# Optimization experiments

Hardware: AMD Instinct MI355X
Metric: run time of the kernel (lower is better)

The kernel has to match this reference:

```python
import jax, jax.numpy as jnp
import numpy as np

S, B, T = 400, 32, 32          # encoder seq len, batch, max_summary_length
V, OOV, E, H = 50000, 50, 128, 256


def _p(key, shape, scale=0.05):
    return (jax.random.normal(key, shape) * scale).astype(jnp.float32)


def lstm_step(x, h, c, Wih, Whh, bih, bhh):
    # PyTorch LSTM gate order: i, f, g, o
    g = x @ Wih.T + h @ Whh.T + bih + bhh
    i, f, gg, o = jnp.split(g, 4, axis=-1)
    c = jax.nn.sigmoid(f) * c + jax.nn.sigmoid(i) * jnp.tanh(gg)
    h = jax.nn.sigmoid(o) * jnp.tanh(c)
    return h, c


def setup_inputs() -> dict:
    key = jax.random.key(0)
    ks = jax.random.split(key, 34)
    inp = {
        # token ids >= 1 so encoder_mask = clip(inputs,0,1) is all ones and
        # packed lengths == full length (PackedRNN becomes a plain LSTM)
        "inputs": jax.random.randint(ks[0], (S, B), 1, V),
        "inputs_lengths": jnp.full((B,), S, dtype=jnp.int32),
        "outputs_tokens": jax.random.randint(ks[1], (T, B), 1, V),  # teacher-forced targets
        "texts_extended": jax.random.randint(ks[2], (S, B), 1, V + OOV),
        "oov_size": OOV,
        # learned parameters
        "embedding": _p(ks[3], (V, E)).at[0].set(0.0),  # padding_idx=0
        "enc_Wih_f": _p(ks[4], (4 * H, E)), "enc_Whh_f": _p(ks[5], (4 * H, H)),
        "enc_bih_f": _p(ks[6], (4 * H,)), "enc_bhh_f": _p(ks[7], (4 * H,)),
        "enc_Wih_b": _p(ks[8], (4 * H, E)), "enc_Whh_b": _p(ks[9], (4 * H, H)),
        "enc_bih_b": _p(ks[10], (4 * H,)), "enc_bhh_b": _p(ks[11], (4 * H,)),
        "W_feat": _p(ks[12], (2 * H, 2 * H)),  # encoder.features (no bias)
        "W_rh": _p(ks[13], (H, 2 * H)), "b_rh": _p(ks[14], (H,)),
        "W_rc": _p(ks[15], (H, 2 * H)), "b_rc": _p(ks[16], (H,)),
        "W_af": _p(ks[17], (2 * H, 2 * H)), "b_af": _p(ks[18], (2 * H,)),  # attention.features
        "w_v": _p(ks[19], (2 * H,)),  # attention_first Linear(2H,1,no bias)
        "W_ctx": _p(ks[20], (E, 2 * H + E)), "b_ctx": _p(ks[21], (E,)),  # decoder.context
        "dec_Wih": _p(ks[22], (4 * H, E)), "dec_Whh": _p(ks[23], (4 * H, H)),
        "dec_bih": _p(ks[24], (4 * H,)), "dec_bhh": _p(ks[25], (4 * H,)),
        "W_pg": _p(ks[26], (1, 4 * H + E)), "b_pg": _p(ks[27], (1,)),
        "W_o1": _p(ks[28], (H, 4 * H)), "b_o1": _p(ks[29], (H,)),
        "W_o2": _p(ks[30], (V, H)), "b_o2": _p(ks[31], (V,)),
    }
    return inp


def reference(inputs, inputs_lengths, outputs_tokens, texts_extended, oov_size,
              embedding, enc_Wih_f, enc_Whh_f, enc_bih_f, enc_bhh_f,
              enc_Wih_b, enc_Whh_b, enc_bih_b, enc_bhh_b,
              W_feat, W_rh, b_rh, W_rc, b_rc, W_af, b_af, w_v,
              W_ctx, b_ctx, dec_Wih, dec_Whh, dec_bih, dec_bhh,
              W_pg, b_pg, W_o1, b_o1, W_o2, b_o2):
    Bsz = inputs.shape[1]
    emb_in = embedding[inputs]                                # [S,B,E]
    h0 = jnp.zeros((Bsz, H), jnp.float32)

    # --- bidirectional encoder LSTM (lengths == S, so packing is a no-op) ---
    def enc_f(carry, x):
        h, c = carry
        h, c = lstm_step(x, h, c, enc_Wih_f, enc_Whh_f, enc_bih_f, enc_bhh_f)
        return (h, c), h

    def enc_b(carry, x):
        h, c = carry
        h, c = lstm_step(x, h, c, enc_Wih_b, enc_Whh_b, enc_bih_b, enc_bhh_b)
        return (h, c), h

    (hf, cf), out_f = jax.lax.scan(enc_f, (h0, h0), emb_in)
    (hb, cb), out_b = jax.lax.scan(enc_b, (h0, h0), emb_in[::-1])
    out_b = out_b[::-1]
    enc_out = jnp.concatenate([out_f, out_b], -1)             # [S,B,2H]
    enc_feat = enc_out @ W_feat.T                             # [S,B,2H]
    dh0 = jax.nn.relu(jnp.concatenate([hf, hb], -1) @ W_rh.T + b_rh)  # [B,H]
    dc0 = jax.nn.relu(jnp.concatenate([cf, cb], -1) @ W_rc.T + b_rc)  # [B,H]

    mask = jnp.clip(inputs, 0, 1).astype(jnp.float32)          # [S,B]
    ctx0 = jnp.zeros((Bsz, 2 * H), jnp.float32)
    rows = jnp.arange(Bsz)[:, None]
    tex_T = texts_extended.T                                   # [B,S]

    # --- decoder loop (teacher forcing, coverage disabled: default) ---
    def dec_step(carry, tok):
        h, c, ctx = carry
        x = jnp.concatenate([ctx, embedding[tok]], 1) @ W_ctx.T + b_ctx     # [B,E]
        h, c = lstm_step(x, h, c, dec_Wih, dec_Whh, dec_bih, dec_bhh)
        dh = jnp.concatenate([h, c], 1)                                      # [B,2H]
        e = jnp.tanh(enc_feat + (dh @ W_af.T + b_af)[None]) @ w_v            # [S,B]
        a = jax.nn.softmax(e, axis=0) * mask
        a = a / a.sum(0, keepdims=True)                                      # layers.Normalize(0)
        context = jnp.einsum('sb,sbd->bd', a, enc_out)                       # [B,2H]
        p_gen = jax.nn.sigmoid(jnp.concatenate([context, dh, x], 1) @ W_pg.T + b_pg)  # [B,1]
        hid = jnp.concatenate([dh, context], 1) @ W_o1.T + b_o1              # [B,H]
        out_v = jax.nn.softmax(hid @ W_o2.T + b_o2, axis=1)                  # [B,V]
        vd = jnp.pad(p_gen * out_v, ((0, 0), (0, oov_size)))                 # [B,V+OOV]
        final = vd.at[rows, tex_T].add((1.0 - p_gen) * a.T)                  # scatter_add copy dist
        return (h, c, context), (final, a)

    _, (outs, atts) = jax.lax.scan(dec_step, (dh0, dc0, ctx0), outputs_tokens)
    return outs, atts  # [T,B,V+OOV], [T,S,B]
```

## Files before the change

### kernel.cpp

```cpp
#include <hip/hip_runtime.h>

#define DEV static __device__ __forceinline__

typedef short  s16x8 __attribute__((ext_vector_type(8)));
typedef float  f32x4 __attribute__((ext_vector_type(4)));
typedef _Float16 h2f __attribute__((ext_vector_type(2)));

constexpr int S = 400, B = 32, T = 32, V = 50000, OOV = 50, E = 128, H = 256;
constexpr int VO = V + OOV, SB = S * B;
constexpr int VP = 50048;

DEV ushort f2bf(float x) {
    union { float f; unsigned u; } a; a.f = x;
    unsigned r = (a.u + 0x7fffu + ((a.u >> 16) & 1u)) >> 16;
    return (ushort)r;
}
DEV float bf2f(unsigned b) {
    union { unsigned u; float f; } a; a.u = b << 16; return a.f;
}
DEV float sigmoidf_(float x) { return 1.0f / (1.0f + __expf(-x)); }
DEV float tanhf_(float x) { float e = __expf(2.0f * x); return 1.0f - 2.0f / (e + 1.0f); }
DEV h2f asH2(unsigned u) { union { unsigned u; h2f h; } x; x.u = u; return x.h; }

#if __has_builtin(__builtin_amdgcn_fdot2)
DEV float dot2(h2f a, h2f b, float c) { return __builtin_amdgcn_fdot2(a, b, c, false); }
#else
DEV float dot2(h2f a, h2f b, float c) { return c + (float)a.x * (float)b.x + (float)a.y * (float)b.y; }
#endif

DEV unsigned f2e4(float v) {
    union { float f; unsigned u; } a; a.f = v;
    unsigned u = a.u + 0x0007FFFFu + ((a.u >> 20) & 1u);
    int e = (int)((u >> 23) & 255) - 127 + 7;
    unsigned m = (u >> 20) & 7u;
    if (e <= 0) return 0u;
    if (e > 15) { e = 15; m = 6; }
    return (unsigned)((e << 3) | m);
}
DEV float e42f(unsigned b) {
    int e = (int)((b >> 3) & 15), m = (int)(b & 7);
    if (e == 0) return (float)m * 1.953125e-3f;
    union { unsigned u; float f; } a;
    a.u = ((unsigned)(e + 120) << 23) | ((unsigned)m << 20);
    return a.f;
}

constexpr size_t SZ_EMB2D  = (size_t)SB * E * 2;
constexpr size_t SZ_WIHCAT = (size_t)2048 * 128 * 2;
constexpr size_t SZ_BIASX  = 2048 * 4;
constexpr size_t SZ_WFEAT  = (size_t)512 * 512 * 2;
constexpr size_t SZ_WO2    = (size_t)V * H * 2;
constexpr size_t SZ_WHH2   = (size_t)2 * 64 * 512 * 16;
constexpr size_t SZ_WCAT   = (size_t)1024 * 896 * 4;
constexpr size_t SZ_BC     = 1024 * 4;
constexpr size_t SZ_CPG    = 256;
constexpr size_t SZ_WRHT   = (size_t)512 * 256 * 4;
constexpr size_t SZ_WRCT   = (size_t)512 * 256 * 4;
constexpr size_t SZ_EMBDEC = (size_t)T * B * E * 4;
constexpr size_t SZ_WZ     = 1664 * 4 + 256;
constexpr size_t SZ_WAFBF  = (size_t)512 * 512 * 2;
constexpr size_t SZ_WO1BF  = (size_t)256 * 1024 * 2;
constexpr size_t SZ_CTXACC = (size_t)(T + 2) * 16384 * 4;
constexpr size_t SZ_SSUM   = (size_t)(T + 2) * 32 * 4 + 256;
constexpr size_t SZ_XALL   = (size_t)T * B * 1024 * 2;
constexpr size_t SZ_EXPS   = (size_t)T * SB * 4;
constexpr size_t SZ_XPROJ  = (size_t)SB * 2048 * 2;
constexpr size_t SZ_ENCOUT = (size_t)SB * 512 * 2;
constexpr size_t SZ_ENCFEAT= (size_t)SB * 512 * 2;
constexpr size_t SZ_HFIN   = (size_t)2 * B * H * 4;
constexpr size_t SZ_HPP    = (size_t)2 * B * H * 4;
constexpr size_t SZ_PGEN   = (size_t)T * B * 4;
constexpr size_t SZ_HIDALL = (size_t)T * B * 256 * 2;

constexpr size_t OFF_EMB2D  = 0;
constexpr size_t OFF_WIHCAT = OFF_EMB2D  + SZ_EMB2D;
constexpr size_t OFF_BIASX  = OFF_WIHCAT + SZ_WIHCAT;
constexpr size_t OFF_WFEAT  = OFF_BIASX  + SZ_BIASX;
constexpr size_t OFF_WO2    = OFF_WFEAT  + SZ_WFEAT;
constexpr size_t OFF_WHH2   = OFF_WO2    + SZ_WO2;
constexpr size_t OFF_WCAT   = OFF_WHH2   + SZ_WHH2;
constexpr size_t OFF_BC     = OFF_WCAT   + SZ_WCAT;
constexpr size_t OFF_CPG    = OFF_BC     + SZ_BC;
constexpr size_t OFF_WRHT   = OFF_CPG    + SZ_CPG;
constexpr size_t OFF_WRCT   = OFF_WRHT   + SZ_WRHT;
constexpr size_t OFF_EMBDEC = OFF_WRCT   + SZ_WRCT;
constexpr size_t OFF_WZ     = OFF_EMBDEC + SZ_EMBDEC;
constexpr size_t OFF_WAFBF  = OFF_WZ     + SZ_WZ;
constexpr size_t OFF_WO1BF  = OFF_WAFBF  + SZ_WAFBF;
constexpr size_t OFF_CTXACC = OFF_WO1BF  + SZ_WO1BF;
constexpr size_t OFF_SSUM   = OFF_CTXACC + SZ_CTXACC;
constexpr size_t OFF_XALL   = OFF_SSUM   + SZ_SSUM;
constexpr size_t OFF_EXPS   = OFF_XALL   + SZ_XALL;
constexpr size_t OFF_XPROJ  = OFF_EXPS   + SZ_EXPS;
constexpr size_t OFF_ENCOUT = OFF_XPROJ  + SZ_XPROJ;
constexpr size_t OFF_ENCFEAT= OFF_ENCOUT + SZ_ENCOUT;
constexpr size_t OFF_HFIN   = OFF_ENCFEAT+ SZ_ENCFEAT;
constexpr size_t OFF_CFIN   = OFF_HFIN   + SZ_HFIN;
constexpr size_t OFF_HPP    = OFF_CFIN   + SZ_HFIN;
constexpr size_t OFF_CPP    = OFF_HPP    + SZ_HPP;
constexpr size_t OFF_PGEN   = OFF_CPP    + SZ_HPP;
constexpr size_t OFF_HIDALL = OFF_PGEN   + SZ_PGEN;
constexpr size_t OFF_PBUF   = OFF_XPROJ;

constexpr long P1 = 2048L*128;
constexpr long P2 = 2048;
constexpr long P3 = 512L*512;
constexpr long P4 = (long)V*H;
constexpr long P5 = 2L*64*512*4;
constexpr long P6 = 1024L*896;
constexpr long P7 = 1;
constexpr long P8 = 1024;
constexpr long P9 = (long)SB*E;
constexpr long P10 = 512L*256;
constexpr long P11 = 512L*256;
constexpr long P12 = 32L*32*128;
constexpr long P13 = 1664;
constexpr long P14 = 512L*512;
constexpr long P15 = 256L*1024;
constexpr long P16 = (long)(T+2)*16384;
constexpr long P17 = (long)(T+2)*32;
constexpr long PREP_TOTAL = P1+P2+P3+P4+P5+P6+P7+P8+P9+P10+P11+P12+P13+P14+P15+P16+P17;

__global__ __launch_bounds__(256)
void prep_kernel(const float* __restrict__ Wih_f, const float* __restrict__ Wih_b,
                 const float* __restrict__ bih_f, const float* __restrict__ bhh_f,
                 const float* __restrict__ bih_b, const float* __restrict__ bhh_b,
                 const float* __restrict__ W_feat, const float* __restrict__ W_o2,
                 const float* __restrict__ Whh_f, const float* __restrict__ Whh_b,
                 const float* __restrict__ dWih, const float* __restrict__ W_ctx,
                 const float* __restrict__ W_pg, const float* __restrict__ b_pg,
                 const float* __restrict__ b_ctx, const float* __restrict__ dbih,
                 const float* __restrict__ dbhh, const float* __restrict__ emb,
                 const int* __restrict__ inputs, const float* __restrict__ dWhh,
                 const float* __restrict__ W_rh, const float* __restrict__ W_rc,
                 const int* __restrict__ toks, const float* __restrict__ W_af,
                 const float* __restrict__ W_o1,
                 ushort* __restrict__ emb2d, ushort* __restrict__ wihcat,
                 float* __restrict__ biasx, ushort* __restrict__ wfeatbf,
                 ushort* __restrict__ wo2bf, unsigned* __restrict__ whh2,
                 float* __restrict__ wcat, float* __restrict__ cpgp,
                 float* __restrict__ bcv, float* __restrict__ wrhT,
                 float* __restrict__ wrcT, float* __restrict__ embdec,
                 float* __restrict__ wz, ushort* __restrict__ wafbf,
                 ushort* __restrict__ wo1bf, float* __restrict__ ctxAcc,
                 float* __restrict__ ssumAll)
{
    long id = (long)blockIdx.x * 256 + threadIdx.x;
    if (id < P1) { int r = id >> 7, e = id & 127;
        float v = (r < 1024) ? Wih_f[r*128+e] : Wih_b[(r-1024)*128+e];
        wihcat[id] = f2bf(v); return; }
    id -= P1;
    if (id < P2) { biasx[id] = (id < 1024) ? bih_f[id]+bhh_f[id] : bih_b[id-1024]+bhh_b[id-1024]; return; }
    id -= P2;
    if (id < P3) { wfeatbf[id] = f2bf(W_feat[id]); return; }
    id -= P3;
    if (id < P4) { wo2bf[id] = f2bf(W_o2[id]); return; }
    id -= P4;
    if (id < P5) {
        int q = id & 3; long r = id >> 2;
        int t = (int)(r & 511); r >>= 9; int c = (int)(r & 63); int dir = (int)(r >> 6);
        int gate = c >> 4, p = c & 15, kh = t & 1;
        int j = t >> 1;
        int k0 = kh * 128 + p * 8 + 2 * q;
        int row = gate * 256 + j;
        const float* W = dir ? Whh_b : Whh_f;
        h2f hv; hv.x = (_Float16)W[(size_t)row*256 + k0]; hv.y = (_Float16)W[(size_t)row*256 + k0 + 1];
        whh2[id] = __builtin_bit_cast(unsigned, hv); return; }
    id -= P5;
    if (id < P6) { int col = (int)(id / 896), k = (int)(id % 896);
        if (k < 640) {
            float acc = 0.f;
            for (int e = 0; e < 128; ++e) acc += dWih[col*128+e] * W_ctx[e*640+k];
            wcat[id] = acc;
        } else wcat[id] = dWhh[(size_t)col*256 + (k - 640)];
        return; }
    id -= P6;
    if (id < P7) { float acc = b_pg[0];
        for (int e = 0; e < 128; ++e) acc += W_pg[1024+e] * b_ctx[e];
        cpgp[0] = acc; return; }
    id -= P7;
    if (id < P8) { float acc = dbih[id] + dbhh[id];
        for (int e = 0; e < 128; ++e) acc += dWih[id*128+e] * b_ctx[e];
        bcv[id] = acc; return; }
    id -= P8;
    if (id < P9) { long sb = id >> 7; int e = id & 127;
        emb2d[id] = f2bf(emb[(size_t)inputs[sb]*128 + e]); return; }
    id -= P9;
    if (id < P10) { int j = id & 255; long k = id >> 8;
        wrhT[id] = W_rh[(size_t)j * 512 + k]; return; }
    id -= P10;
    if (id < P11) { int j = id & 255; long k = id >> 8;
        wrcT[id] = W_rc[(size_t)j * 512 + k]; return; }
    id -= P11;
    if (id < P12) { long tb = id >> 7; int e = id & 127;
        embdec[id] = emb[(size_t)toks[tb]*128 + e]; return; }
    id -= P12;
    if (id < P13) {
        int k = (int)id;
        if (k < 1024) wz[k] = W_pg[k];
        else { int u = k - 1024; float acc = 0.f;
            for (int e = 0; e < 128; ++e) acc += W_pg[1024+e] * W_ctx[e*640+u];
            wz[k] = acc; }
        return; }
    id -= P13;
    if (id < P14) { int d = id & 511; long k = id >> 9;
        wafbf[id] = f2bf(W_af[(size_t)d * 512 + k]); return; }
    id -= P14;
    if (id < P15) { wo1bf[id] = f2bf(W_o1[id]); return; }
    id -= P15;
    if (id < P16) { ctxAcc[id] = 0.f; return; }
    id -= P16;
    if (id < P17) { ssumAll[id] = (id < 64) ? 1.0f : 0.f; return; }
}

template<int BM, int BN, int NT, int MODE, bool BIAS, bool SWZ>
__global__ __launch_bounds__(NT)
void gemm_nt(const ushort* __restrict__ A, int lda, const ushort* __restrict__ Bm, int ldb,
             void* __restrict__ Cp, int ldc, const float* __restrict__ bias,
             int M, int N, int K)
{
    constexpr int WN = BN / 32;
    __shared__ ushort sA[BM * 32];
    __shared__ ushort sB[BN * 32];
    int tid = threadIdx.x, lane = tid & 63, wid = tid >> 6;
    int wm = wid / WN, wn = wid % WN;
    int mb = blockIdx.y, nb = blockIdx.x;
    if (SWZ) {
        int n = gridDim.x, x = nb & 7, y = nb >> 3, q = n >> 3, r = n & 7;
// ... 66 lines not shown
    for (int c = 46; c < 64; ++c) wlds[(c - 46) * 512 + t] = gw[(size_t)c * 512];
    if (t < 256) { hh16[0][t >> 7][t & 127] = 0; }
    float cst = 0.f, hst = 0.f;
    __syncthreads();
    const int khoff = kh * 512;
    #pragma unroll 1
    for (int step = 0; step < S; ++step) {
        int s = dir ? (S - 1 - step) : step;
        int cur = step & 1, nxt = cur ^ 1;
        const ushort* xp = xproj + ((size_t)(s * B + b)) * 2048 + dir * 1024 + j + khoff;
        ushort xra = xp[0], xrb = xp[256];
        float a0 = 0.f, a1 = 0.f, a2 = 0.f, a3 = 0.f;
        #pragma unroll
        for (int p = 0; p < 16; ++p) {
            uint4 hp = *(const uint4*)(&hh16[cur][kh][p * 8]);
            uint4 wi = wreg[p];
            uint4 wf = wreg[16 + p];
            uint4 wg = (p < 14) ? wreg[32 + p] : wlds[(p - 14) * 512 + t];
            uint4 wo = wlds[(p + 2) * 512 + t];
            h2f p0 = asH2(hp.x), p1 = asH2(hp.y), p2 = asH2(hp.z), p3 = asH2(hp.w);
            a0 = dot2(p0, asH2(wi.x), a0); a0 = dot2(p1, asH2(wi.y), a0);
            a0 = dot2(p2, asH2(wi.z), a0); a0 = dot2(p3, asH2(wi.w), a0);
            a1 = dot2(p0, asH2(wf.x), a1); a1 = dot2(p1, asH2(wf.y), a1);
            a1 = dot2(p2, asH2(wf.z), a1); a1 = dot2(p3, asH2(wf.w), a1);
            a2 = dot2(p0, asH2(wg.x), a2); a2 = dot2(p1, asH2(wg.y), a2);
            a2 = dot2(p2, asH2(wg.z), a2); a2 = dot2(p3, asH2(wg.w), a2);
            a3 = dot2(p0, asH2(wo.x), a3); a3 = dot2(p1, asH2(wo.y), a3);
            a3 = dot2(p2, asH2(wo.z), a3); a3 = dot2(p3, asH2(wo.w), a3);
        }
        float xv0 = (float)__builtin_bit_cast(_Float16, xra);
        float xv1 = (float)__builtin_bit_cast(_Float16, xrb);
        a0 += kh ? 0.f : xv0;  a1 += kh ? 0.f : xv1;
        a2 += kh ? xv0 : 0.f;  a3 += kh ? xv1 : 0.f;
        a0 += __shfl_xor(a0, 1); a1 += __shfl_xor(a1, 1);
        a2 += __shfl_xor(a2, 1); a3 += __shfl_xor(a3, 1);
        cst = sigmoidf_(a1) * cst + sigmoidf_(a0) * tanhf_(a2);
        hst = sigmoidf_(a3) * tanhf_(cst);
        if (kh == 0) {
            encoutB[((size_t)(b * S + s)) * 512 + dir * 256 + j] = f2bf(hst);
            hh16[nxt][j >> 7][j & 127] = __builtin_bit_cast(ushort, (_Float16)hst);
        }
        __syncthreads();
    }
    if (kh == 0) {
        hfin[(dir * 32 + b) * 256 + j] = hst;
        cfin[(dir * 32 + b) * 256 + j] = cst;
    }
}

__global__ __launch_bounds__(256)
void initdec_kernel(const float* __restrict__ hfin, const float* __restrict__ cfin,
                    const float* __restrict__ wrhT, const float* __restrict__ b_rh,
                    const float* __restrict__ wrcT, const float* __restrict__ b_rc,
                    float* __restrict__ hPP, float* __restrict__ cPP)
{
    int b = blockIdx.x, j = threadIdx.x;
    float ah = b_rh[j], ac = b_rc[j];
    for (int k = 0; k < 512; ++k) {
        float hv = (k < 256) ? hfin[b * 256 + k] : hfin[(32 + b) * 256 + k - 256];
        float cv = (k < 256) ? cfin[b * 256 + k] : cfin[(32 + b) * 256 + k - 256];
        ah += hv * wrhT[k * 256 + j];
        ac += cv * wrcT[k * 256 + j];
    }
    hPP[b * 256 + j] = fmaxf(ah, 0.f);
    cPP[b * 256 + j] = fmaxf(ac, 0.f);
}

__global__ __launch_bounds__(256)
void dec_lstm2_kernel(const float* __restrict__ wcat, const float* __restrict__ bcv,
                      const float* __restrict__ ctxPrevAcc, const float* __restrict__ ssumPrev,
                      const float* __restrict__ hin, const float* __restrict__ cin,
                      float* __restrict__ hout, float* __restrict__ cout,
                      const float* __restrict__ embt, ushort* __restrict__ xAll_t)
{
    __shared__ float pre[256];
    int blk = blockIdx.x, tid = threadIdx.x;
    int b = tid & 31, ci = tid >> 5;
    int gi = ci >> 1, jj = ci & 1;
    int j = (blk << 1) + jj;
    int col = gi * 256 + j;
    float rinvb = 1.0f / ssumPrev[b];
    float acc = bcv[col], accC = 0.f;
    const float4* w = (const float4*)(wcat + (size_t)col * 896);
    const float4* x0 = (const float4*)(ctxPrevAcc + b * 512);
    #pragma unroll 8
    for (int u = 0; u < 128; ++u) { float4 a = w[u], q = x0[u]; accC += a.x*q.x + a.y*q.y + a.z*q.z + a.w*q.w; }
    const float4* x1 = (const float4*)(embt + b * 128);
    #pragma unroll 8
    for (int u = 0; u < 32; ++u) { float4 a = w[128 + u], q = x1[u]; acc += a.x*q.x + a.y*q.y + a.z*q.z + a.w*q.w; }
    const float4* x2 = (const float4*)(hin + b * 256);
    #pragma unroll 8
    for (int u = 0; u < 64; ++u) { float4 a = w[160 + u], q = x2[u]; acc += a.x*q.x + a.y*q.y + a.z*q.z + a.w*q.w; }
    pre[tid] = acc + rinvb * accC;
    __syncthreads();
    if (tid < 64) {
        int b2 = tid & 31, qq = tid >> 5;
        int j2 = (blk << 1) + qq;
        float iv = pre[(0 + qq) * 32 + b2];
        float fv = pre[(2 + qq) * 32 + b2];
        float gv = pre[(4 + qq) * 32 + b2];
        float ov = pre[(6 + qq) * 32 + b2];
        float cp = cin[b2 * 256 + j2];
        float cn = sigmoidf_(fv) * cp + sigmoidf_(iv) * tanhf_(gv);
        float hn = sigmoidf_(ov) * tanhf_(cn);
        cout[b2 * 256 + j2] = cn;
        hout[b2 * 256 + j2] = hn;
        xAll_t[(size_t)b2 * 1024 + j2] = f2bf(hn);
        xAll_t[(size_t)b2 * 1024 + 256 + j2] = f2bf(cn);
    }
}

__global__ __launch_bounds__(512)
void dec_attn2_kernel(const float* __restrict__ h, const float* __restrict__ c,
                      const ushort* __restrict__ wafbf, const float* __restrict__ b_af,
                      const ushort* __restrict__ encfeatB, const float* __restrict__ wv,
                      const int* __restrict__ inputs, const ushort* __restrict__ encoutB,
                      float* __restrict__ expsT, float* __restrict__ ssumT,
                      float* __restrict__ ctxAccT)
{
    __shared__ float hc[512];
    __shared__ float dafL[512];
    __shared__ float scL[50];
    __shared__ float part8[8][512];
    int blk = blockIdx.x, tid = threadIdx.x;
    int b = blk >> 3, sc = blk & 7, s0 = sc * 50;
    int sl = tid >> 6, dth = tid & 63;
    hc[tid] = (tid < 256) ? h[b * 256 + tid] : c[b * 256 + tid - 256];
    __syncthreads();
    {
        float acc8[8] = {};
        const ushort* wbase = wafbf + (size_t)(sl * 64) * 512 + dth * 8;
        #pragma unroll 8
        for (int kk = 0; kk < 64; ++kk) {
            uint4 u = *(const uint4*)(wbase + (size_t)kk * 512);
            float hk = hc[sl * 64 + kk];
            acc8[0] += hk * bf2f(u.x & 0xffffu);
            acc8[1] += hk * bf2f(u.x >> 16);
            acc8[2] += hk * bf2f(u.y & 0xffffu);
            acc8[3] += hk * bf2f(u.y >> 16);
            acc8[4] += hk * bf2f(u.z & 0xffffu);
            acc8[5] += hk * bf2f(u.z >> 16);
            acc8[6] += hk * bf2f(u.w & 0xffffu);
            acc8[7] += hk * bf2f(u.w >> 16);
        }
        #pragma unroll
        for (int jj = 0; jj < 8; ++jj) part8[sl][dth * 8 + jj] = acc8[jj];
    }
    __syncthreads();
    {
        float v = b_af[tid];
        #pragma unroll
        for (int w8 = 0; w8 < 8; ++w8) v += part8[w8][tid];
        dafL[tid] = v;
    }
    __syncthreads();
    float dreg[8], wreg[8];
    #pragma unroll
    for (int jj = 0; jj < 8; ++jj) { dreg[jj] = dafL[dth * 8 + jj]; wreg[jj] = wv[dth * 8 + jj]; }
    for (int i = sl; i < 50; i += 8) {
        int s = s0 + i;
        uint4 u = *(const uint4*)(encfeatB + ((size_t)b * S + s) * 512 + dth * 8);
        h2f e0 = asH2(u.x), e1 = asH2(u.y), e2 = asH2(u.z), e3 = asH2(u.w);
        float e = tanhf_((float)e0.x + dreg[0]) * wreg[0] + tanhf_((float)e0.y + dreg[1]) * wreg[1]
                + tanhf_((float)e1.x + dreg[2]) * wreg[2] + tanhf_((float)e1.y + dreg[3]) * wreg[3]
                + tanhf_((float)e2.x + dreg[4]) * wreg[4] + tanhf_((float)e2.y + dreg[5]) * wreg[5]
                + tanhf_((float)e3.x + dreg[6]) * wreg[6] + tanhf_((float)e3.y + dreg[7]) * wreg[7];
        e += __shfl_xor(e, 1);  e += __shfl_xor(e, 2);
        e += __shfl_xor(e, 4);  e += __shfl_xor(e, 8);
        e += __shfl_xor(e, 16); e += __shfl_xor(e, 32);
        if (dth == 0) {
            float m = (inputs[s * 32 + b] != 0) ? 1.f : 0.f;
            float val = m * __expf(e);
            scL[i] = val;
            expsT[s * 32 + b] = val;
        }
    }
    __syncthreads();
    if (tid == 0) {
        float ss = 0.f;
        for (int i = 0; i < 50; ++i) ss += scL[i];
        atomicAdd(&ssumT[b], ss);
    }
    {
        float acc8[8] = {};
        for (int i = sl; i < 50; i += 8) {
            float a = scL[i];
            uint4 u = *(const uint4*)(encoutB + ((size_t)b * S + s0 + i) * 512 + dth * 8);
            acc8[0] += a * bf2f(u.x & 0xffffu);
            acc8[1] += a * bf2f(u.x >> 16);
            acc8[2] += a * bf2f(u.y & 0xffffu);
            acc8[3] += a * bf2f(u.y >> 16);
            acc8[4] += a * bf2f(u.z & 0xffffu);
            acc8[5] += a * bf2f(u.z >> 16);
            acc8[6] += a * bf2f(u.w & 0xffffu);
            acc8[7] += a * bf2f(u.w >> 16);
        }
        #pragma unroll
        for (int jj = 0; jj < 8; ++jj) part8[sl][dth * 8 + jj] = acc8[jj];
    }
    __syncthreads();
    {
        float v = 0.f;
        #pragma unroll
        for (int s8 = 0; s8 < 8; ++s8) v += part8[s8][tid];
        atomicAdd(&ctxAccT[b * 512 + tid], v);
    }
}

__global__ __launch_bounds__(256)
void cvt_kernel(const float* __restrict__ ctxAcc, const float* __restrict__ ssumAll,
                ushort* __restrict__ xAll)
{
    int id = blockIdx.x * 256 + threadIdx.x;
    int t = id >> 14, rem = id & 16383;
    int b = rem >> 9, k = rem & 511;
    float v = ctxAcc[(size_t)(2 + t) * 16384 + rem] / ssumAll[(2 + t) * 32 + b];
    xAll[(size_t)(t * 32 + b) * 1024 + 512 + k] = f2bf(v);
}

__global__ __launch_bounds__(256)
void pgen_kernel(const ushort* __restrict__ xAll, const float* __restrict__ ctxAcc,
                 const float* __restrict__ ssumAll, const float* __restrict__ embdec,
                 const float* __restrict__ wz, const float* __restrict__ cpgp,
                 float* __restrict__ pgenAll)
{
    int row = blockIdx.x * 8 + (threadIdx.x >> 5);
    int sub = threadIdx.x & 31;
    int t = row >> 5, b = row & 31;
    float rT = 1.0f / ssumAll[(2 + t) * 32 + b];
    float rP = 1.0f / ssumAll[(1 + t) * 32 + b];
    const float* cT = ctxAcc + (size_t)(2 + t) * 16384 + b * 512;
    const float* cP = ctxAcc + (size_t)(1 + t) * 16384 + b * 512;
    const ushort* hx = xAll + (size_t)row * 1024;
    const float* em = embdec + (size_t)row * 128;
    float acc = 0.f;
    for (int k = sub; k < 1664; k += 32) {
        float zv;
        if (k < 512)        zv = cT[k] * rT;
        else if (k < 1024)  zv = bf2f(hx[k - 512]);
        else if (k < 1536)  zv = cP[k - 1024] * rP;
        else                zv = em[k - 1536];
        acc += wz[k] * zv;
    }
    acc += __shfl_xor(acc, 1); acc += __shfl_xor(acc, 2);
    acc += __shfl_xor(acc, 4); acc += __shfl_xor(acc, 8);
    acc += __shfl_xor(acc, 16);
    if (sub == 0) pgenAll[row] = sigmoidf_(acc + cpgp[0]);
}

__global__ __launch_bounds__(256)
void dec_out3_kernel(const unsigned char* __restrict__ pbuf, const float* __restrict__ pgenAll,
                     const int* __restrict__ tex, const float* __restrict__ expsAll,
                     const float* __restrict__ ssumAll,
                     float* __restrict__ outsAll, float* __restrict__ attsAll)
{
    int tb = blockIdx.x, t = threadIdx.x;
    int tstep = tb >> 5, b = tb & 31;
    const unsigned char* prow = pbuf + (size_t)tb * VP;
    float part = 0.f;
    for (int i = t; i < V / 8; i += 256) {
        uint2 u = *(const uint2*)(prow + i * 8);
        unsigned w0 = u.x, w1 = u.y;
        part += e42f(w0 & 255) + e42f((w0 >> 8) & 255) + e42f((w0 >> 16) & 255) + e42f(w0 >> 24);
        part += e42f(w1 & 255) + e42f((w1 >> 8) & 255) + e42f((w1 >> 16) & 255) + e42f(w1 >> 24);
    }
    __shared__ float red[256];
    red[t] = part;
    __syncthreads();
    for (int o = 128; o > 0; o >>= 1) { if (t < o) red[t] += red[t + o]; __syncthreads(); }
    float pg = pgenAll[tb];
    float sca = pg / red[0];
    float om = 1.f - pg;
    float rinv = 1.0f / ssumAll[(2 + tstep) * 32 + b];
    float* orow = outsAll + (size_t)tstep * B * VO + (size_t)b * VO;
    for (int i = t; i < V / 8; i += 256) {
        uint2 u = *(const uint2*)(prow + i * 8);
        unsigned w0 = u.x, w1 = u.y;
        float2* o2 = (float2*)(orow + i * 8);
        o2[0] = make_float2(e42f(w0 & 255) * sca, e42f((w0 >> 8) & 255) * sca);
        o2[1] = make_float2(e42f((w0 >> 16) & 255) * sca, e42f(w0 >> 24) * sca);
        o2[2] = make_float2(e42f(w1 & 255) * sca, e42f((w1 >> 8) & 255) * sca);
        o2[3] = make_float2(e42f((w1 >> 16) & 255) * sca, e42f(w1 >> 24) * sca);
    }
    if (t < OOV) orow[V + t] = 0.f;
    __syncthreads();
    const float* expst = expsAll + (size_t)tstep * SB;
    float* attst = attsAll + (size_t)tstep * SB;
    for (int si = t; si < 400; si += 256) {
        float an = expst[si * 32 + b] * rinv;
        attst[si * 32 + b] = an;
        atomicAdd(orow + tex[si * 32 + b], om * an);
    }
}

extern "C" void kernel_launch(void* const* d_in, const int* in_sizes, int n_in,
                              void* d_out, int out_size, void* d_ws, size_t ws_size,
                              hipStream_t stream)
{
    const int*   inputs  = (const int*)d_in[0];
    const int*   toksAll = (const int*)d_in[2];
    const int*   tex     = (const int*)d_in[3];
    const float* emb     = (const float*)d_in[5];
    const float* Wih_f   = (const float*)d_in[6];
    const float* Whh_f   = (const float*)d_in[7];
    const float* bih_f   = (const float*)d_in[8];
    const float* bhh_f   = (const float*)d_in[9];
    const float* Wih_b   = (const float*)d_in[10];
    const float* Whh_b   = (const float*)d_in[11];
    const float* bih_b   = (const float*)d_in[12];
    const float* bhh_b   = (const float*)d_in[13];
    const float* W_feat  = (const float*)d_in[14];
    const float* W_rh    = (const float*)d_in[15];
    const float* b_rh    = (const float*)d_in[16];
    const float* W_rc    = (const float*)d_in[17];
    const float* b_rc    = (const float*)d_in[18];
    const float* W_af    = (const float*)d_in[19];
    const float* b_af    = (const float*)d_in[20];
    const float* w_v     = (const float*)d_in[21];
    const float* W_ctx   = (const float*)d_in[22];
    const float* b_ctx   = (const float*)d_in[23];
    const float* dWih    = (const float*)d_in[24];
    const float* dWhh    = (const float*)d_in[25];
    const float* dbih    = (const float*)d_in[26];
    const float* dbhh    = (const float*)d_in[27];
    const float* W_pg    = (const float*)d_in[28];
    const float* b_pg    = (const float*)d_in[29];
    const float* W_o1    = (const float*)d_in[30];
    const float* b_o1    = (const float*)d_in[31];
    const float* W_o2    = (const float*)d_in[32];
    const float* b_o2    = (const float*)d_in[33];

    char* wsb = (char*)d_ws;
    ushort*   emb2d   = (ushort*)(wsb + OFF_EMB2D);
    ushort*   wihcat  = (ushort*)(wsb + OFF_WIHCAT);
    float*    biasx   = (float*)(wsb + OFF_BIASX);
    ushort*   wfeatbf = (ushort*)(wsb + OFF_WFEAT);
    ushort*   wo2bf   = (ushort*)(wsb + OFF_WO2);
    unsigned* whh2    = (unsigned*)(wsb + OFF_WHH2);
    float*    wcat    = (float*)(wsb + OFF_WCAT);
    float*    bcv     = (float*)(wsb + OFF_BC);
    float*    cpgp    = (float*)(wsb + OFF_CPG);
    float*    wrhT    = (float*)(wsb + OFF_WRHT);
    float*    wrcT    = (float*)(wsb + OFF_WRCT);
    float*    embdec  = (float*)(wsb + OFF_EMBDEC);
    float*    wz      = (float*)(wsb + OFF_WZ);
    ushort*   wafbf   = (ushort*)(wsb + OFF_WAFBF);
    ushort*   wo1bf   = (ushort*)(wsb + OFF_WO1BF);
    float*    ctxAcc  = (float*)(wsb + OFF_CTXACC);
    float*    ssumAll = (float*)(wsb + OFF_SSUM);
    ushort*   xAll    = (ushort*)(wsb + OFF_XALL);
    float*    expsAll = (float*)(wsb + OFF_EXPS);
    ushort*   xproj   = (ushort*)(wsb + OFF_XPROJ);
    ushort*   encoutB = (ushort*)(wsb + OFF_ENCOUT);
    ushort*   encfeatB= (ushort*)(wsb + OFF_ENCFEAT);
    float*    hfin    = (float*)(wsb + OFF_HFIN);
    float*    cfin    = (float*)(wsb + OFF_CFIN);
    float*    hPP     = (float*)(wsb + OFF_HPP);
    float*    cPP     = (float*)(wsb + OFF_CPP);
    float*    pgenAll = (float*)(wsb + OFF_PGEN);
    ushort*   hidAll  = (ushort*)(wsb + OFF_HIDALL);
    unsigned char* pbuf = (unsigned char*)(wsb + OFF_PBUF);

    float* outs = (float*)d_out;
    float* atts = outs + (size_t)T * B * VO;

    int prep_blocks = (int)((PREP_TOTAL + 255) / 256);
    prep_kernel<<<prep_blocks, 256, 0, stream>>>(
        Wih_f, Wih_b, bih_f, bhh_f, bih_b, bhh_b, W_feat, W_o2, Whh_f, Whh_b,
        dWih, W_ctx, W_pg, b_pg, b_ctx, dbih, dbhh, emb, inputs, dWhh, W_rh, W_rc,
        toksAll, W_af, W_o1,
        emb2d, wihcat, biasx, wfeatbf, wo2bf, whh2, wcat, cpgp, bcv, wrhT, wrcT,
        embdec, wz, wafbf, wo1bf, ctxAcc, ssumAll);

    gemm_nt<64, 64, 256, 1, true, false><<<dim3(2048 / 64, SB / 64), 256, 0, stream>>>(
        emb2d, 128, wihcat, 128, (void*)xproj, 2048, biasx, SB, 2048, 128);

    enc_kernel<<<64, 512, 0, stream>>>(xproj, (const uint4*)whh2, encoutB, hfin, cfin);

    initdec_kernel<<<32, 256, 0, stream>>>(hfin, cfin, wrhT, b_rh, wrcT, b_rc, hPP, cPP);

    gemm_nt<64, 64, 256, 1, false, false><<<dim3(512 / 64, SB / 64), 256, 0, stream>>>(
        encoutB, 512, wfeatbf, 512, (void*)encfeatB, 512, nullptr, SB, 512, 512);

    for (int t = 0; t < T; ++t) {
        int p = t & 1, q = p ^ 1;
        float* hin = hPP + (size_t)p * 8192;
        float* cin = cPP + (size_t)p * 8192;
        float* hout = hPP + (size_t)q * 8192;
        float* cout = cPP + (size_t)q * 8192;
        dec_lstm2_kernel<<<128, 256, 0, stream>>>(
            wcat, bcv,
            ctxAcc + (size_t)(t + 1) * 16384, ssumAll + (t + 1) * 32,
            hin, cin, hout, cout,
            embdec + (size_t)t * 4096, xAll + (size_t)t * 32768);
        dec_attn2_kernel<<<256, 512, 0, stream>>>(
            hout, cout, wafbf, b_af, encfeatB, w_v, inputs, encoutB,
            expsAll + (size_t)t * SB, ssumAll + (2 + t) * 32,
            ctxAcc + (size_t)(2 + t) * 16384);
    }
    cvt_kernel<<<(T * B * 512) / 256, 256, 0, stream>>>(ctxAcc, ssumAll, xAll);
    pgen_kernel<<<128, 256, 0, stream>>>(xAll, ctxAcc, ssumAll, embdec, wz, cpgp, pgenAll);
    gemm_nt<64, 64, 256, 3, true, false><<<dim3(256 / 64, 1024 / 64), 256, 0, stream>>>(
        xAll, 1024, wo1bf, 1024, (void*)hidAll, 256, b_o1, T * B, 256, 1024);
    gemm_nt<64, 128, 512, 4, true, true><<<dim3(391, 16), 512, 0, stream>>>(
        hidAll, 256, wo2bf, 256, (void*)pbuf, VP, b_o2, T * B, V, 256);
    dec_out3_kernel<<<T * B, 256, 0, stream>>>(pbuf, pgenAll, tex, expsAll, ssumAll, outs, atts);
}
```

Baseline: 2.876 ms.

## Fuse decoder time loop into one persistent per-batch kernel

The 64 per-step launches of the decoder LSTM and attention kernels are replaced by a single persistent kernel with one 1024-thread block per batch row. That block keeps h, c and the context in shared memory across all 32 steps, removing launch overhead, inter-kernel round trips and atomics. The combined LSTM weight is repacked as fp16 pairs in k-major layout so adjacent threads read coalesced columns. The cost is that only 32 blocks run, so each block rereads the full LSTM and attention weights every step with little GPU parallelism. The fp16 weights also lower precision.

```diff
diff --git a/kernel.cpp b/kernel.cpp
--- a/kernel.cpp
+++ b/kernel.cpp
@@ -18,6 +18,7 @@
 DEV float bf2f(unsigned b) {
     union { unsigned u; float f; } a; a.u = b << 16; return a.f;
 }
+DEV float f16f(unsigned u16) { return (float)__builtin_bit_cast(_Float16, (ushort)u16); }
 DEV float sigmoidf_(float x) { return 1.0f / (1.0f + __expf(-x)); }
 DEV float tanhf_(float x) { float e = __expf(2.0f * x); return 1.0f - 2.0f / (e + 1.0f); }
 DEV h2f asH2(unsigned u) { union { unsigned u; h2f h; } x; x.u = u; return x.h; }
@@ -51,7 +52,7 @@
 constexpr size_t SZ_WFEAT  = (size_t)512 * 512 * 2;
 constexpr size_t SZ_WO2    = (size_t)V * H * 2;
 constexpr size_t SZ_WHH2   = (size_t)2 * 64 * 512 * 16;
-constexpr size_t SZ_WCAT   = (size_t)1024 * 896 * 4;
+constexpr size_t SZ_WLSTM2 = (size_t)896 * 512 * 4;
 constexpr size_t SZ_BC     = 1024 * 4;
 constexpr size_t SZ_CPG    = 256;
 constexpr size_t SZ_WRHT   = (size_t)512 * 256 * 4;
@@ -63,12 +64,12 @@
 constexpr size_t SZ_CTXACC = (size_t)(T + 2) * 16384 * 4;
 constexpr size_t SZ_SSUM   = (size_t)(T + 2) * 32 * 4 + 256;
 constexpr size_t SZ_XALL   = (size_t)T * B * 1024 * 2;
-constexpr size_t SZ_EXPS   = (size_t)T * SB * 4;
+constexpr size_t SZ_EXPS   = (size_t)(T + 1) * SB * 4;
 constexpr size_t SZ_XPROJ  = (size_t)SB * 2048 * 2;
 constexpr size_t SZ_ENCOUT = (size_t)SB * 512 * 2;
 constexpr size_t SZ_ENCFEAT= (size_t)SB * 512 * 2;
 constexpr size_t SZ_HFIN   = (size_t)2 * B * H * 4;
-constexpr size_t SZ_HPP    = (size_t)2 * B * H * 4;
+constexpr size_t SZ_H0     = (size_t)B * H * 4;
 constexpr size_t SZ_PGEN   = (size_t)T * B * 4;
 constexpr size_t SZ_HIDALL = (size_t)T * B * 256 * 2;
 
@@ -78,8 +79,8 @@
 constexpr size_t OFF_WFEAT  = OFF_BIASX  + SZ_BIASX;
 constexpr size_t OFF_WO2    = OFF_WFEAT  + SZ_WFEAT;
 constexpr size_t OFF_WHH2   = OFF_WO2    + SZ_WO2;
-constexpr size_t OFF_WCAT   = OFF_WHH2   + SZ_WHH2;
-constexpr size_t OFF_BC     = OFF_WCAT   + SZ_WCAT;
+constexpr size_t OFF_WLSTM2 = OFF_WHH2   + SZ_WHH2;
+constexpr size_t OFF_BC     = OFF_WLSTM2 + SZ_WLSTM2;
 constexpr size_t OFF_CPG    = OFF_BC     + SZ_BC;
 constexpr size_t OFF_WRHT   = OFF_CPG    + SZ_CPG;
 constexpr size_t OFF_WRCT   = OFF_WRHT   + SZ_WRHT;
@@ -96,9 +97,9 @@
 constexpr size_t OFF_ENCFEAT= OFF_ENCOUT + SZ_ENCOUT;
 constexpr size_t OFF_HFIN   = OFF_ENCFEAT+ SZ_ENCFEAT;
 constexpr size_t OFF_CFIN   = OFF_HFIN   + SZ_HFIN;
-constexpr size_t OFF_HPP    = OFF_CFIN   + SZ_HFIN;
-constexpr size_t OFF_CPP    = OFF_HPP    + SZ_HPP;
-constexpr size_t OFF_PGEN   = OFF_CPP    + SZ_HPP;
+constexpr size_t OFF_H0     = OFF_CFIN   + SZ_HFIN;
+constexpr size_t OFF_C0     = OFF_H0     + SZ_H0;
+constexpr size_t OFF_PGEN   = OFF_C0     + SZ_H0;
 constexpr size_t OFF_HIDALL = OFF_PGEN   + SZ_PGEN;
 constexpr size_t OFF_PBUF   = OFF_XPROJ;
 
@@ -107,7 +108,7 @@
 constexpr long P3 = 512L*512;
 constexpr long P4 = (long)V*H;
 constexpr long P5 = 2L*64*512*4;
-constexpr long P6 = 1024L*896;
+constexpr long P6 = 896L*512;
 constexpr long P7 = 1;
 constexpr long P8 = 1024;
 constexpr long P9 = (long)SB*E;
@@ -138,7 +139,7 @@
                  ushort* __restrict__ emb2d, ushort* __restrict__ wihcat,
                  float* __restrict__ biasx, ushort* __restrict__ wfeatbf,
                  ushort* __restrict__ wo2bf, unsigned* __restrict__ whh2,
-                 float* __restrict__ wcat, float* __restrict__ cpgp,
+                 unsigned* __restrict__ wlstm2, float* __restrict__ cpgp,
                  float* __restrict__ bcv, float* __restrict__ wrhT,
                  float* __restrict__ wrcT, float* __restrict__ embdec,
                  float* __restrict__ wz, ushort* __restrict__ wafbf,
@@ -167,13 +168,24 @@
         h2f hv; hv.x = (_Float16)W[(size_t)row*256 + k0]; hv.y = (_Float16)W[(size_t)row*256 + k0 + 1];
         whh2[id] = __builtin_bit_cast(unsigned, hv); return; }
     id -= P5;
-    if (id < P6) { int col = (int)(id / 896), k = (int)(id % 896);
+    if (id < P6) {
+        int c = (int)(id & 511), k = (int)(id >> 9);
+        float v0, v1;
         if (k < 640) {
-            float acc = 0.f;
-            for (int e = 0; e < 128; ++e) acc += dWih[col*128+e] * W_ctx[e*640+k];
-            wcat[id] = acc;
-        } else wcat[id] = dWhh[(size_t)col*256 + (k - 640)];
-        return; }
+            float a0 = 0.f, a1 = 0.f;
+            for (int e = 0; e < 128; ++e) {
+                float wc = W_ctx[e * 640 + k];
+                a0 += dWih[c * 128 + e] * wc;
+                a1 += dWih[(c + 512) * 128 + e] * wc;
+            }
+            v0 = a0; v1 = a1;
+        } else {
+            v0 = dWhh[(size_t)c * 256 + (k - 640)];
+            v1 = dWhh[(size_t)(c + 512) * 256 + (k - 640)];
+        }
+        unsigned lo = (unsigned)__builtin_bit_cast(ushort, (_Float16)v0);
+        unsigned hi = (unsigned)__builtin_bit_cast(ushort, (_Float16)v1);
+        wlstm2[id] = lo | (hi << 16); return; }
     id -= P6;
     if (id < P7) { float acc = b_pg[0];
         for (int e = 0; e < 128; ++e) acc += W_pg[1024+e] * b_ctx[e];
@@ -346,7 +358,7 @@
 void initdec_kernel(const float* __restrict__ hfin, const float* __restrict__ cfin,
                     const float* __restrict__ wrhT, const float* __restrict__ b_rh,
                     const float* __restrict__ wrcT, const float* __restrict__ b_rc,
-                    float* __restrict__ hPP, float* __restrict__ cPP)
+                    float* __restrict__ h0, float* __restrict__ c0)
 {
     int b = blockIdx.x, j = threadIdx.x;
     float ah = b_rh[j], ac = b_rc[j];
@@ -356,148 +368,157 @@
         ah += hv * wrhT[k * 256 + j];
         ac += cv * wrcT[k * 256 + j];
     }
-    hPP[b * 256 + j] = fmaxf(ah, 0.f);
-    cPP[b * 256 + j] = fmaxf(ac, 0.f);
-}
-
-__global__ __launch_bounds__(256)
-void dec_lstm2_kernel(const float* __restrict__ wcat, const float* __restrict__ bcv,
-                      const float* __restrict__ ctxPrevAcc, const float* __restrict__ ssumPrev,
-                      const float* __restrict__ hin, const float* __restrict__ cin,
-                      float* __restrict__ hout, float* __restrict__ cout,
-                      const float* __restrict__ embt, ushort* __restrict__ xAll_t)
-{
-    __shared__ float pre[256];
-    int blk = blockIdx.x, tid = threadIdx.x;
-    int b = tid & 31, ci = tid >> 5;
-    int gi = ci >> 1, jj = ci & 1;
-    int j = (blk << 1) + jj;
-    int col = gi * 256 + j;
-    float rinvb = 1.0f / ssumPrev[b];
-    float acc = bcv[col], accC = 0.f;
-    const float4* w = (const float4*)(wcat + (size_t)col * 896);
-    const float4* x0 = (const float4*)(ctxPrevAcc + b * 512);
-    #pragma unroll 8
-    for (int u = 0; u < 128; ++u) { float4 a = w[u], q = x0[u]; accC += a.x*q.x + a.y*q.y + a.z*q.z + a.w*q.w; }
-    const float4* x1 = (const float4*)(embt + b * 128);
-    #pragma unroll 8
-    for (int u = 0; u < 32; ++u) { float4 a = w[128 + u], q = x1[u]; acc += a.x*q.x + a.y*q.y + a.z*q.z + a.w*q.w; }
-    const float4* x2 = (const float4*)(hin + b * 256);
-    #pragma unroll 8
-    for (int u = 0; u < 64; ++u) { float4 a = w[160 + u], q = x2[u]; acc += a.x*q.x + a.y*q.y + a.z*q.z + a.w*q.w; }
-    pre[tid] = acc + rinvb * accC;
-    __syncthreads();
-    if (tid < 64) {
-        int b2 = tid & 31, qq = tid >> 5;
-        int j2 = (blk << 1) + qq;
-        float iv = pre[(0 + qq) * 32 + b2];
-        float fv = pre[(2 + qq) * 32 + b2];
-        float gv = pre[(4 + qq) * 32 + b2];
-        float ov = pre[(6 + qq) * 32 + b2];
-        float cp = cin[b2 * 256 + j2];
-        float cn = sigmoidf_(fv) * cp + sigmoidf_(iv) * tanhf_(gv);
-        float hn = sigmoidf_(ov) * tanhf_(cn);
-        cout[b2 * 256 + j2] = cn;
-        hout[b2 * 256 + j2] = hn;
-        xAll_t[(size_t)b2 * 1024 + j2] = f2bf(hn);
-        xAll_t[(size_t)b2 * 1024 + 256 + j2] = f2bf(cn);
-    }
-}
-
-__global__ __launch_bounds__(512)
-void dec_attn2_kernel(const float* __restrict__ h, const float* __restrict__ c,
-                      const ushort* __restrict__ wafbf, const float* __restrict__ b_af,
-                      const ushort* __restrict__ encfeatB, const float* __restrict__ wv,
-                      const int* __restrict__ inputs, const ushort* __restrict__ encoutB,
-                      float* __restrict__ expsT, float* __restrict__ ssumT,
-                      float* __restrict__ ctxAccT)
-{
-    __shared__ float hc[512];
+    h0[b * 256 + j] = fmaxf(ah, 0.f);
+    c0[b * 256 + j] = fmaxf(ac, 0.f);
+}
+
+__global__ __launch_bounds__(1024)
+void decloop_kernel(const unsigned* __restrict__ wlstm2, const float* __restrict__ bcv,
+                    const float* __restrict__ embdec,
+                    const float* __restrict__ h0, const float* __restrict__ c0,
+                    const ushort* __restrict__ wafbf, const float* __restrict__ b_af,
+                    const ushort* __restrict__ encfeatB, const float* __restrict__ wv,
+                    const int* __restrict__ inputs, const ushort* __restrict__ encoutB,
+                    ushort* __restrict__ xAll, float* __restrict__ expsAll,
+                    float* __restrict__ ssumAll, float* __restrict__ ctxAcc)
+{
+    __shared__ float xv[896];
+    __shared__ float gl2[2][1024];
+    __shared__ float hcL[512];
     __shared__ float dafL[512];
-    __shared__ float scL[50];
-    __shared__ float part8[8][512];
-    int blk = blockIdx.x, tid = threadIdx.x;
-    int b = blk >> 3, sc = blk & 7, s0 = sc * 50;
-    int sl = tid >> 6, dth = tid & 63;
-    hc[tid] = (tid < 256) ? h[b * 256 + tid] : c[b * 256 + tid - 256];
-    __syncthreads();
-    {
-        float acc8[8] = {};
-        const ushort* wbase = wafbf + (size_t)(sl * 64) * 512 + dth * 8;
-        #pragma unroll 8
-        for (int kk = 0; kk < 64; ++kk) {
-            uint4 u = *(const uint4*)(wbase + (size_t)kk * 512);
-            float hk = hc[sl * 64 + kk];
-            acc8[0] += hk * bf2f(u.x & 0xffffu);
-            acc8[1] += hk * bf2f(u.x >> 16);
-            acc8[2] += hk * bf2f(u.y & 0xffffu);
-            acc8[3] += hk * bf2f(u.y >> 16);
-            acc8[4] += hk * bf2f(u.z & 0xffffu);
-            acc8[5] += hk * bf2f(u.z >> 16);
-            acc8[6] += hk * bf2f(u.w & 0xffffu);
-            acc8[7] += hk * bf2f(u.w >> 16);
-        }
+    __shared__ float scL[400];
+    __shared__ float part16[16][512];
+    __shared__ float red[512];
+    __shared__ float ssumL;
+    int b = blockIdx.x, tid = threadIdx.x;
+    int cid = tid & 511, kh = tid >> 9;
+    int dth = tid & 63, sl = tid >> 6;
+    if (tid < 512) xv[tid] = 0.f;
+    else if (tid < 768) { int j = tid - 512; float hv = h0[b * 256 + j]; hcL[j] = hv; xv[640 + j] = hv; }
+    else { int j = tid - 768; hcL[256 + j] = c0[b * 256 + j]; }
+    float wreg[8];
+    #pragma unroll
+    for (int jj = 0; jj < 8; ++jj) wreg[jj] = wv[dth * 8 + jj];
+
+    for (int t = 0; t < T; ++t) {
+        if (tid >= 512 && tid < 640)
+            xv[tid] = embdec[(size_t)t * 4096 + b * 128 + (tid - 512)];
+        __syncthreads();
+        {
+            float a0 = 0.f, a1 = 0.f, a0b = 0.f, a1b = 0.f;
+            const unsigned* wk = wlstm2 + (size_t)(kh * 448) * 512 + cid;
+            const float* xk = xv + kh * 448;
+            #pragma unroll 8
+            for (int k = 0; k < 448; k += 2) {
+                unsigned u0 = wk[(size_t)k * 512];
+                unsigned u1 = wk[(size_t)(k + 1) * 512];
+                float x0 = xk[k], x1 = xk[k + 1];
+                a0  += x0 * f16f(u0 & 0xffffu);
+                a1  += x0 * f16f(u0 >> 16);
+                a0b += x1 * f16f(u1 & 0xffffu);
+                a1b += x1 * f16f(u1 >> 16);
+            }
+            gl2[kh][cid] = a0 + a0b;
+            gl2[kh][512 + cid] = a1 + a1b;
+        }
+        __syncthreads();
+        if (tid < 256) {
+            int j = tid;
+            float gi = gl2[0][j]       + gl2[1][j]       + bcv[j];
+            float gf = gl2[0][256 + j] + gl2[1][256 + j] + bcv[256 + j];
+            float gg = gl2[0][512 + j] + gl2[1][512 + j] + bcv[512 + j];
+            float go = gl2[0][768 + j] + gl2[1][768 + j] + bcv[768 + j];
+            float cp = hcL[256 + j];
+            float cn = sigmoidf_(gf) * cp + sigmoidf_(gi) * tanhf_(gg);
+            float hn = sigmoidf_(go) * tanhf_(cn);
+            hcL[j] = hn; hcL[256 + j] = cn;
+            xv[640 + j] = hn;
+            xAll[((size_t)t * 32 + b) * 1024 + j] = f2bf(hn);
+            xAll[((size_t)t * 32 + b) * 1024 + 256 + j] = f2bf(cn);
+        }
+        __syncthreads();
+        {
+            float acc8[8] = {};
+            const ushort* wbase = wafbf + (size_t)(sl * 32) * 512 + dth * 8;
+            #pragma unroll 8
+            for (int kk = 0; kk < 32; ++kk) {
+                uint4 u = *(const uint4*)(wbase + (size_t)kk * 512);
+                float hk = hcL[sl * 32 + kk];
+                acc8[0] += hk * bf2f(u.x & 0xffffu);
+                acc8[1] += hk * bf2f(u.x >> 16);
+                acc8[2] += hk * bf2f(u.y & 0xffffu);
+                acc8[3] += hk * bf2f(u.y >> 16);
+                acc8[4] += hk * bf2f(u.z & 0xffffu);
+                acc8[5] += hk * bf2f(u.z >> 16);
+                acc8[6] += hk * bf2f(u.w & 0xffffu);
+                acc8[7] += hk * bf2f(u.w >> 16);
+            }
+            #pragma unroll
+            for (int jj = 0; jj < 8; ++jj) part16[sl][dth * 8 + jj] = acc8[jj];
+        }
+        __syncthreads();
+        if (tid < 512) {
+            float v = b_af[tid];
+            #pragma unroll
+            for (int i = 0; i < 16; ++i) v += part16[i][tid];
+            dafL[tid] = v;
+        }
+        __syncthreads();
+        float dreg[8];
         #pragma unroll
-        for (int jj = 0; jj < 8; ++jj) part8[sl][dth * 8 + jj] = acc8[jj];
-    }
-    __syncthreads();
-    {
-        float v = b_af[tid];
-        #pragma unroll
-        for (int w8 = 0; w8 < 8; ++w8) v += part8[w8][tid];
-        dafL[tid] = v;
-    }
-    __syncthreads();
-    float dreg[8], wreg[8];
-    #pragma unroll
-    for (int jj = 0; jj < 8; ++jj) { dreg[jj] = dafL[dth * 8 + jj]; wreg[jj] = wv[dth * 8 + jj]; }
-    for (int i = sl; i < 50; i += 8) {
-        int s = s0 + i;
-        uint4 u = *(const uint4*)(encfeatB + ((size_t)b * S + s) * 512 + dth * 8);
-        h2f e0 = asH2(u.x), e1 = asH2(u.y), e2 = asH2(u.z), e3 = asH2(u.w);
-        float e = tanhf_((float)e0.x + dreg[0]) * wreg[0] + tanhf_((float)e0.y + dreg[1]) * wreg[1]
-                + tanhf_((float)e1.x + dreg[2]) * wreg[2] + tanhf_((float)e1.y + dreg[3]) * wreg[3]
-                + tanhf_((float)e2.x + dreg[4]) * wreg[4] + tanhf_((float)e2.y + dreg[5]) * wreg[5]
-                + tanhf_((float)e3.x + dreg[6]) * wreg[6] + tanhf_((float)e3.y + dreg[7]) * wreg[7];
-        e += __shfl_xor(e, 1);  e += __shfl_xor(e, 2);
-        e += __shfl_xor(e, 4);  e += __shfl_xor(e, 8);
-        e += __shfl_xor(e, 16); e += __shfl_xor(e, 32);
-        if (dth == 0) {
-            float m = (inputs[s * 32 + b] != 0) ? 1.f : 0.f;
-            float val = m * __expf(e);
-            scL[i] = val;
-            expsT[s * 32 + b] = val;
-        }
-    }
-    __syncthreads();
-    if (tid == 0) {
-        float ss = 0.f;
-        for (int i = 0; i < 50; ++i) ss += scL[i];
-        atomicAdd(&ssumT[b], ss);
-    }
-    {
-        float acc8[8] = {};
-        for (int i = sl; i < 50; i += 8) {
-            float a = scL[i];
-            uint4 u = *(const uint4*)(encoutB + ((size_t)b * S + s0 + i) * 512 + dth * 8);
-            acc8[0] += a * bf2f(u.x & 0xffffu);
-            acc8[1] += a * bf2f(u.x >> 16);
-            acc8[2] += a * bf2f(u.y & 0xffffu);
-            acc8[3] += a * bf2f(u.y >> 16);
-            acc8[4] += a * bf2f(u.z & 0xffffu);
-            acc8[5] += a * bf2f(u.z >> 16);
-            acc8[6] += a * bf2f(u.w & 0xffffu);
-            acc8[7] += a * bf2f(u.w >> 16);
-        }
-        #pragma unroll
-        for (int jj = 0; jj < 8; ++jj) part8[sl][dth * 8 + jj] = acc8[jj];
-    }
-    __syncthreads();
-    {
-        float v = 0.f;
-        #pragma unroll
-        for (int s8 = 0; s8 < 8; ++s8) v += part8[s8][tid];
-        atomicAdd(&ctxAccT[b * 512 + tid], v);
+        for (int jj = 0; jj < 8; ++jj) dreg[jj] = dafL[dth * 8 + jj];
+        for (int i = 0; i < 25; ++i) {
+            int s = sl + i * 16;
+            uint4 u = *(const uint4*)(encfeatB + ((size_t)b * S + s) * 512 + dth * 8);
+            h2f e0 = asH2(u.x), e1 = asH2(u.y), e2 = asH2(u.z), e3 = asH2(u.w);
+            float e = tanhf_((float)e0.x + dreg[0]) * wreg[0] + tanhf_((float)e0.y + dreg[1]) * wreg[1]
+                    + tanhf_((float)e1.x + dreg[2]) * wreg[2] + tanhf_((float)e1.y + dreg[3]) * wreg[3]
+                    + tanhf_((float)e2.x + dreg[4]) * wreg[4] + tanhf_((float)e2.y + dreg[5]) * wreg[5]
+                    + tanhf_((float)e3.x + dreg[6]) * wreg[6] + tanhf_((float)e3.y + dreg[7]) * wreg[7];
+            e += __shfl_xor(e, 1);  e += __shfl_xor(e, 2);
+            e += __shfl_xor(e, 4);  e += __shfl_xor(e, 8);
+            e += __shfl_xor(e, 16); e += __shfl_xor(e, 32);
+            if (dth == 0) {
+                float m = (inputs[s * 32 + b] != 0) ? 1.f : 0.f;
+                float val = m * __expf(e);
+                scL[s] = val;
+                expsAll[(size_t)(1 + t) * SB + s * 32 + b] = val;
+            }
+        }
+        __syncthreads();
+        if (tid < 512) red[tid] = (tid < 400) ? scL[tid] : 0.f;
+        __syncthreads();
+        for (int o = 256; o > 0; o >>= 1) { if (tid < o) red[tid] += red[tid + o]; __syncthreads(); }
+        if (tid == 0) { ssumL = red[0]; ssumAll[(2 + t) * 32 + b] = red[0]; }
+        __syncthreads();
+        float rinv = 1.0f / ssumL;
+        {
+            float acc8[8] = {};
+            for (int i = 0; i < 25; ++i) {
+                int s = sl + i * 16;
+                float a = scL[s];
+                uint4 u = *(const uint4*)(encoutB + ((size_t)b * S + s) * 512 + dth * 8);
+                acc8[0] += a * bf2f(u.x & 0xffffu);
+                acc8[1] += a * bf2f(u.x >> 16);
+                acc8[2] += a * bf2f(u.y & 0xffffu);
+                acc8[3] += a * bf2f(u.y >> 16);
+                acc8[4] += a * bf2f(u.z & 0xffffu);
+                acc8[5] += a * bf2f(u.z >> 16);
+                acc8[6] += a * bf2f(u.w & 0xffffu);
+                acc8[7] += a * bf2f(u.w >> 16);
+            }
+            #pragma unroll
+            for (int jj = 0; jj < 8; ++jj) part16[sl][dth * 8 + jj] = acc8[jj];
+        }
+        __syncthreads();
+        if (tid < 512) {
+            float v = 0.f;
+            #pragma unroll
+            for (int i = 0; i < 16; ++i) v += part16[i][tid];
+            ctxAcc[(size_t)(2 + t) * 16384 + (size_t)b * 512 + tid] = v;
+            xv[tid] = v * rinv;
+        }
+        __syncthreads();
     }
 }
 
@@ -578,7 +599,7 @@
     }
     if (t < OOV) orow[V + t] = 0.f;
     __syncthreads();
-    const float* expst = expsAll + (size_t)tstep * SB;
+    const float* expst = expsAll + (size_t)(1 + tstep) * SB;
     float* attst = attsAll + (size_t)tstep * SB;
     for (int si = t; si < 400; si += 256) {
         float an = expst[si * 32 + b] * rinv;
@@ -631,7 +652,7 @@
     ushort*   wfeatbf = (ushort*)(wsb + OFF_WFEAT);
     ushort*   wo2bf   = (ushort*)(wsb + OFF_WO2);
     unsigned* whh2    = (unsigned*)(wsb + OFF_WHH2);
-    float*    wcat    = (float*)(wsb + OFF_WCAT);
+    unsigned* wlstm2  = (unsigned*)(wsb + OFF_WLSTM2);
     float*    bcv     = (float*)(wsb + OFF_BC);
     float*    cpgp    = (float*)(wsb + OFF_CPG);
     float*    wrhT    = (float*)(wsb + OFF_WRHT);
@@ -649,8 +670,8 @@
     ushort*   encfeatB= (ushort*)(wsb + OFF_ENCFEAT);
     float*    hfin    = (float*)(wsb + OFF_HFIN);
     float*    cfin    = (float*)(wsb + OFF_CFIN);
-    float*    hPP     = (float*)(wsb + OFF_HPP);
-    float*    cPP     = (float*)(wsb + OFF_CPP);
+    float*    h0      = (float*)(wsb + OFF_H0);
+    float*    c0      = (float*)(wsb + OFF_C0);
     float*    pgenAll = (float*)(wsb + OFF_PGEN);
     ushort*   hidAll  = (ushort*)(wsb + OFF_HIDALL);
     unsigned char* pbuf = (unsigned char*)(wsb + OFF_PBUF);
@@ -663,7 +684,7 @@
         Wih_f, Wih_b, bih_f, bhh_f, bih_b, bhh_b, W_feat, W_o2, Whh_f, Whh_b,
         dWih, W_ctx, W_pg, b_pg, b_ctx, dbih, dbhh, emb, inputs, dWhh, W_rh, W_rc,
         toksAll, W_af, W_o1,
-        emb2d, wihcat, biasx, wfeatbf, wo2bf, whh2, wcat, cpgp, bcv, wrhT, wrcT,
+        emb2d, wihcat, biasx, wfeatbf, wo2bf, whh2, wlstm2, cpgp, bcv, wrhT, wrcT,
         embdec, wz, wafbf, wo1bf, ctxAcc, ssumAll);
 
     gemm_nt<64, 64, 256, 1, true, false><<<dim3(2048 / 64, SB / 64), 256, 0, stream>>>(
@@ -671,27 +692,15 @@
 
     enc_kernel<<<64, 512, 0, stream>>>(xproj, (const uint4*)whh2, encoutB, hfin, cfin);
 
-    initdec_kernel<<<32, 256, 0, stream>>>(hfin, cfin, wrhT, b_rh, wrcT, b_rc, hPP, cPP);
+    initdec_kernel<<<32, 256, 0, stream>>>(hfin, cfin, wrhT, b_rh, wrcT, b_rc, h0, c0);
 
     gemm_nt<64, 64, 256, 1, false, false><<<dim3(512 / 64, SB / 64), 256, 0, stream>>>(
         encoutB, 512, wfeatbf, 512, (void*)encfeatB, 512, nullptr, SB, 512, 512);
 
-    for (int t = 0; t < T; ++t) {
-        int p = t & 1, q = p ^ 1;
-        float* hin = hPP + (size_t)p * 8192;
-        float* cin = cPP + (size_t)p * 8192;
-        float* hout = hPP + (size_t)q * 8192;
-        float* cout = cPP + (size_t)q * 8192;
-        dec_lstm2_kernel<<<128, 256, 0, stream>>>(
-            wcat, bcv,
-            ctxAcc + (size_t)(t + 1) * 16384, ssumAll + (t + 1) * 32,
-            hin, cin, hout, cout,
-            embdec + (size_t)t * 4096, xAll + (size_t)t * 32768);
-        dec_attn2_kernel<<<256, 512, 0, stream>>>(
-            hout, cout, wafbf, b_af, encfeatB, w_v, inputs, encoutB,
-            expsAll + (size_t)t * SB, ssumAll + (2 + t) * 32,
-            ctxAcc + (size_t)(2 + t) * 16384);
-    }
+    decloop_kernel<<<32, 1024, 0, stream>>>(
+        wlstm2, bcv, embdec, h0, c0, wafbf, b_af, encfeatB, w_v, inputs, encoutB,
+        xAll, expsAll, ssumAll, ctxAcc);
+
     cvt_kernel<<<(T * B * 512) / 256, 256, 0, stream>>>(ctxAcc, ssumAll, xAll);
     pgen_kernel<<<128, 256, 0, stream>>>(xAll, ctxAcc, ssumAll, embdec, wz, cpgp, pgenAll);
     gemm_nt<64, 64, 256, 3, true, false><<<dim3(256 / 64, 1024 / 64), 256, 0, stream>>>(
```

Result: slower. 5.753 ms (+100.1%).
